# Optimization experiments

Hardware: AMD Instinct MI355X
Metric: run time of the kernel (lower is better)

The kernel has to match this reference:

```python
import jax, jax.numpy as jnp
import numpy as np

N = 10000          # nodes
E = 160000         # edges
T = 32             # seq_len == n_timesteps
H = 256            # hidden_size
K = 4              # edge_embedding_dim
NF = T * 6         # node_features
PRED = 8           # predicted_timesteps
T_TEACH = T - PRED # teacher-forced steps


def setup_inputs() -> dict:
    key = jax.random.key(0)
    ks = jax.random.split(key, 16)
    s = 0.05
    return {
        "x": jax.random.normal(ks[0], (N, NF), jnp.float32),
        "edge_index": jax.random.randint(ks[1], (2, E), 0, N, jnp.int64),
        "z": jax.random.uniform(ks[2], (E, K), jnp.float32),
        # inner f_out: Linear(H, NF) + ReLU
        "Wf": jax.random.normal(ks[3], (H, NF), jnp.float32) * s,
        "bf": jax.random.normal(ks[4], (NF,), jnp.float32) * s,
        # k-1 edge MLPs: Linear(2*NF, H) -> ReLU -> Linear(H, H), stacked
        "W1": jax.random.normal(ks[5], (K - 1, 2 * NF, H), jnp.float32) * s,
        "b1": jax.random.normal(ks[6], (K - 1, H), jnp.float32) * s,
        "W2": jax.random.normal(ks[7], (K - 1, H, H), jnp.float32) * s,
        "b2": jax.random.normal(ks[8], (K - 1, H), jnp.float32) * s,
        # GRUCell(6, H): torch gate order r, z, n
        "Wih": jax.random.normal(ks[9], (3 * H, 6), jnp.float32) * s,
        "bih": jax.random.normal(ks[10], (3 * H,), jnp.float32) * s,
        "Whh": jax.random.normal(ks[11], (3 * H, H), jnp.float32) * s,
        "bhh": jax.random.normal(ks[12], (3 * H,), jnp.float32) * s,
        # outer f_out: Linear(H, 6) + ReLU
        "Wo": jax.random.normal(ks[13], (H, 6), jnp.float32) * s,
        "bo": jax.random.normal(ks[14], (6,), jnp.float32) * s,
    }


def _forward(x, edge_index, z, Wf, bf, W1, b1, W2, b2, Wih, bih, Whh, bhh, Wo, bo):
    src = edge_index[0]  # x_j (source)
    dst = edge_index[1]  # x_i (target, aggregation index)
    zw = z[:, 1:K].T[:, :, None]  # [K-1, E, 1]
    ones_e = jnp.ones((E,), x.dtype)
    cnt = jnp.maximum(jax.ops.segment_sum(ones_e, dst, num_segments=N), 1.0)[:, None]

    def step(carry, inp):
        h, prev = carry
        t, x_t = inp
        inputs = jnp.where(t < T_TEACH, x_t, prev)  # [N, 6]
        fh = jax.nn.relu(h @ Wf + bf)               # [N, NF]
        # message: cat([x_i, x_j]) = [target, source], detached in torch
        ef = jax.lax.stop_gradient(
            jnp.concatenate([fh[dst], fh[src]], axis=1))  # [E, 2*NF]
        h1 = jax.nn.relu(jnp.einsum('ef,kfh->keh', ef, W1) + b1[:, None, :])
        h2 = jnp.einsum('keh,khg->keg', h1, W2) + b2[:, None, :]  # [K-1,E,H]
        msg = jnp.sum(zw * h2, axis=0)              # [E, H]
        m = jax.ops.segment_sum(msg, dst, num_segments=N) / cnt  # scatter-mean
        # GRUCell(inputs, hidden=m)
        gx = inputs @ Wih.T + bih                   # [N, 3H]
        gh = m @ Whh.T + bhh                        # [N, 3H]
        rx, zx, nx = jnp.split(gx, 3, axis=1)
        rh, zh, nh = jnp.split(gh, 3, axis=1)
        r = jax.nn.sigmoid(rx + rh)
        zg = jax.nn.sigmoid(zx + zh)
        n = jnp.tanh(nx + r * nh)
        h_new = (1.0 - zg) * n + zg * m             # [N, H]
        mu = inputs + jax.nn.relu(h_new @ Wo + bo)  # [N, 6]
        return (h_new, mu), mu

    x_seq = x.reshape(N, T, 6).transpose(1, 0, 2)   # [T, N, 6]
    ts = jnp.arange(T)
    h0 = jnp.zeros((N, H), x.dtype)
    p0 = jnp.zeros((N, 6), x.dtype)
    _, mus = jax.lax.scan(step, (h0, p0), (ts, x_seq))  # [T, N, 6]
    return mus.transpose(1, 0, 2).reshape(N, NF)


def reference(x, edge_index, z, Wf, bf, W1, b1, W2, b2, Wih, bih, Whh, bhh, Wo, bo):
    return _forward(x, edge_index, z, Wf, bf, W1, b1, W2, b2,
                    Wih, bih, Whh, bhh, Wo, bo)
```

## Files before the change

kernel.cpp:

```cpp
#include <hip/hip_runtime.h>
#include <hip/hip_bf16.h>

#define NN 10000
#define NE 160000
#define TS 32
#define HID 256
#define NFEAT 192
#define TTEACH 24

typedef unsigned short u16;
typedef unsigned int u32;
typedef __attribute__((ext_vector_type(8))) short bf16x8;
typedef __attribute__((ext_vector_type(4))) float f32x4;

__device__ __forceinline__ float bf2f(u16 u){
    u32 v = ((u32)u) << 16;
    union { u32 i; float f; } c; c.i = v; return c.f;
}
__device__ __forceinline__ u16 f2bf(float f){
    union { float f; u32 i; } c; c.f = f;
    u32 i = c.i;
    u32 lsb = (i >> 16) & 1u;
    i += 0x7fffu + lsb;
    return (u16)(i >> 16);
}

__global__ void fill_f32(float* p, float v, int n){
    int i = blockIdx.x * 256 + threadIdx.x;
    if (i < n) p[i] = v;
}
__global__ void fill_i32(int* p, int v, int n){
    int i = blockIdx.x * 256 + threadIdx.x;
    if (i < n) p[i] = v;
}
__global__ void copy_i32(const int* __restrict__ a, int* __restrict__ b, int n){
    int i = blockIdx.x * 256 + threadIdx.x;
    if (i < n) b[i] = a[i];
}
__global__ void copy_f32(const float* __restrict__ a, float* __restrict__ b, int n){
    int i = blockIdx.x * 256 + threadIdx.x;
    if (i < n) b[i] = a[i];
}

__global__ void detect_f32(const u16* __restrict__ zraw, int* __restrict__ flag){
    int c = 0;
    for (int i = 0; i < 128; i++) if (zraw[2*i] >= 0x4000) c++;
    *flag = (c > 8) ? 1 : 0;
}
__global__ void conv_f32(const void* __restrict__ in, float* __restrict__ outp,
                         int n, const int* __restrict__ flag){
    int i = blockIdx.x * 256 + threadIdx.x;
    if (i >= n) return;
    if (*flag) outp[i] = ((const float*)in)[i];
    else       outp[i] = bf2f(((const u16*)in)[i]);
}
__global__ void detect_i64(const int* __restrict__ ei_raw, int* __restrict__ flag){
    int zz = 0;
    #pragma unroll
    for (int i = 0; i < 32; i++) zz |= ei_raw[2*i + 1];
    *flag = (zz == 0) ? 1 : 0;
}
__global__ void copy_edges(const int* __restrict__ ei_raw, const int* __restrict__ flag,
                           int* __restrict__ src, int* __restrict__ dst){
    int e = blockIdx.x * 256 + threadIdx.x;
    if (e >= NE) return;
    int st = (*flag) ? 2 : 1;
    src[e] = ei_raw[(size_t)e * st];
    dst[e] = ei_raw[((size_t)NE + e) * st];
}

__global__ void degree_k(const int* __restrict__ dst, int* __restrict__ cnt, int n){
    int e = blockIdx.x * 256 + threadIdx.x;
    if (e < n) atomicAdd(&cnt[dst[e]], 1);
}
__global__ void invcnt_k(const int* __restrict__ cnt, float* __restrict__ inv, int n){
    int i = blockIdx.x * 256 + threadIdx.x;
    if (i < n) inv[i] = 1.0f / fmaxf((float)cnt[i], 1.0f);
}

__global__ void scan_k(const int* __restrict__ cnt, int* __restrict__ binoff){
    __shared__ int ps[1024];
    int t = threadIdx.x;
    int s = 0;
    if (t < 1000)
        for (int i = 0; i < 10; i++) s += cnt[t*10 + i];
    ps[t] = s;
    __syncthreads();
    for (int ofs = 1; ofs < 1024; ofs <<= 1){
        int v = (t >= ofs) ? ps[t - ofs] : 0;
        __syncthreads();
        ps[t] += v;
        __syncthreads();
    }
    if (t < 1000){
        int run = (t == 0) ? 0 : ps[t-1];
        for (int i = 0; i < 10; i++){
            binoff[t*10 + i] = run;
            run += cnt[t*10 + i];
        }
    }
}
__global__ void scatter_k(const int* __restrict__ src32, const int* __restrict__ dst32,
                          const float* __restrict__ zc, int* __restrict__ cur,
                          int* __restrict__ srcS, int* __restrict__ dstS,
                          float* __restrict__ zS){
    int e = blockIdx.x * 256 + threadIdx.x;
    if (e >= NE) return;
    int d = dst32[e];
    int pos = atomicAdd(&cur[d], 1);
    srcS[pos] = src32[e];
    dstS[pos] = d;
    zS[pos]        = zc[(size_t)e*4 + 1];
    zS[NE + pos]   = zc[(size_t)e*4 + 2];
    zS[2*NE + pos] = zc[(size_t)e*4 + 3];
}

__global__ void zsum_k(const int* __restrict__ dst32, const float* __restrict__ zc,
                       float* __restrict__ zsum){
    int e = blockIdx.x * 256 + threadIdx.x;
    if (e >= NE) return;
    int d = dst32[e];
    atomicAdd(&zsum[d*3 + 0], zc[(size_t)e*4 + 1]);
    atomicAdd(&zsum[d*3 + 1], zc[(size_t)e*4 + 2]);
    atomicAdd(&zsum[d*3 + 2], zc[(size_t)e*4 + 3]);
}
__global__ void build_bias_k(const float* __restrict__ zsum, const float* __restrict__ b2c,
                             float* __restrict__ bias_node){
    int idx = blockIdx.x * 256 + threadIdx.x;
    if (idx >= NN * 256) return;
    int n = idx >> 8, c = idx & 255;
    bias_node[idx] = zsum[n*3]*b2c[c] + zsum[n*3+1]*b2c[256+c] + zsum[n*3+2]*b2c[512+c];
}

__global__ void build_wft(const float* __restrict__ Wfc, u16* __restrict__ WfT){
    int idx = blockIdx.x * 256 + threadIdx.x;
    if (idx < 256 * 192){
        int k = idx / 192, n = idx % 192;
        WfT[(size_t)n * 256 + k] = f2bf(Wfc[idx]);
    }
}
__global__ void build_w1t(const float* __restrict__ W1c, u16* __restrict__ W1T){
    int idx = blockIdx.x * 256 + threadIdx.x;
    if (idx < 1536 * 192){
        int n = idx / 192, k = idx % 192;
        int kblk = n >> 9, part = (n >> 8) & 1, c = n & 255;
        W1T[idx] = f2bf(W1c[(size_t)kblk * (384*256) + (size_t)(part*192 + k) * 256 + c]);
    }
}
__global__ void conv_bf16(const float* __restrict__ in, u16* __restrict__ outp, int n){
    int i = blockIdx.x * 256 + threadIdx.x;
    if (i < n) outp[i] = f2bf(in[i]);
}
__global__ void build_w2t(const float* __restrict__ W2c, u16* __restrict__ W2T){
    int idx = blockIdx.x * 256 + threadIdx.x;
    if (idx < 768 * 256){
        int k = idx / 256, n = idx % 256;
        W2T[(size_t)n * 768 + k] = f2bf(W2c[idx]);
    }
}

template<int MODE>
__global__ __launch_bounds__(256, 2) void gemm_mfma(
    const u16* __restrict__ A16, const u16* __restrict__ BT16,
    const float* __restrict__ bias, float* __restrict__ Cf, u16* __restrict__ Cb,
    const float* __restrict__ A32, const float* __restrict__ rowscale,
    int M, int Kd, int Nd)
{
    __shared__ __align__(16) u16 Alds[256 * 40];
    __shared__ __align__(16) u16 Blds[64 * 40];
    const int tid = threadIdx.x;
    const int m0 = blockIdx.x * 256;
    const int n0 = blockIdx.y * 64;
    const int wave = tid >> 6, lane = tid & 63;
    const int quad = lane >> 4, l16 = lane & 15;

    const f32x4 zero4 = {0.f, 0.f, 0.f, 0.f};
    f32x4 acc[4][4];
    #pragma unroll
    for (int r=0;r<4;r++)
        #pragma unroll
        for (int c=0;c<4;c++) acc[r][c] = zero4;

    const int arow = m0 + tid;
    const u16* ap = (MODE == 2) ? nullptr : &A16[(size_t)arow * Kd];
    const int bn = tid >> 2, bseg = tid & 3;
    const u16* bp = &BT16[(size_t)(n0 + bn) * Kd + bseg * 8];
    float rs = 0.f;
    if (MODE == 2 && arow < M) rs = rowscale[arow];

    for (int k0 = 0; k0 < Kd; k0 += 32){
        if (MODE == 2){
            if (arow < M){
                const float4* q = reinterpret_cast<const float4*>(&A32[(size_t)arow * Kd + k0]);
                u32 pk[16];
                #pragma unroll
                for (int s=0;s<8;s++){
                    float4 v = q[s];
                    float2 p0; p0.x = v.x * rs; p0.y = v.y * rs;
                    float2 p1; p1.x = v.z * rs; p1.y = v.w * rs;
                    __hip_bfloat162 h0 = __float22bfloat162_rn(p0);
                    __hip_bfloat162 h1 = __float22bfloat162_rn(p1);
                    pk[2*s]   = *reinterpret_cast<u32*>(&h0);
                    pk[2*s+1] = *reinterpret_cast<u32*>(&h1);
                }
                #pragma unroll
                for (int s=0;s<4;s++)
                    *reinterpret_cast<uint4*>(&Alds[tid * 40 + s*8]) = *reinterpret_cast<uint4*>(&pk[4*s]);
            } else {
                uint4 zz = {0,0,0,0};
                #pragma unroll
                for (int s=0;s<4;s++)
                    *reinterpret_cast<uint4*>(&Alds[tid * 40 + s*8]) = zz;
            }
        } else {
            if (arow < M){
                const uint4* q = reinterpret_cast<const uint4*>(ap + k0);
                uint4 v0 = q[0], v1 = q[1], v2 = q[2], v3 = q[3];
                *reinterpret_cast<uint4*>(&Alds[tid * 40])      = v0;
                *reinterpret_cast<uint4*>(&Alds[tid * 40 + 8])  = v1;
                *reinterpret_cast<uint4*>(&Alds[tid * 40 + 16]) = v2;
                *reinterpret_cast<uint4*>(&Alds[tid * 40 + 24]) = v3;
            } else {
                uint4 zz = {0,0,0,0};
                #pragma unroll
                for (int s=0;s<4;s++)
                    *reinterpret_cast<uint4*>(&Alds[tid * 40 + s*8]) = zz;
            }
        }
        {
            uint4 v = *reinterpret_cast<const uint4*>(bp + k0);
            *reinterpret_cast<uint4*>(&Blds[bn * 40 + bseg * 8]) = v;
        }
        __syncthreads();
        bf16x8 af[4], bfr[4];
        #pragma unroll
        for (int r=0;r<4;r++)
            af[r] = *reinterpret_cast<const bf16x8*>(&Alds[(wave*64 + r*16 + l16) * 40 + quad * 8]);
        #pragma unroll
        for (int c=0;c<4;c++)
            bfr[c] = *reinterpret_cast<const bf16x8*>(&Blds[(c*16 + l16) * 40 + quad * 8]);
        #pragma unroll
        for (int r=0;r<4;r++)
            #pragma unroll
            for (int c=0;c<4;c++)
                acc[r][c] = __builtin_amdgcn_mfma_f32_16x16x32_bf16(af[r], bfr[c], acc[r][c], 0, 0, 0);
        __syncthreads();
    }
    #pragma unroll
    for (int c=0;c<4;c++){
        int col = n0 + c*16 + l16;
        float bv = 0.f;
        if (MODE == 0 || MODE == 2) bv = bias[col];
        if (MODE == 1){
            int part = (col >> 8) & 1;
            if (part == 0) bv = bias[(col >> 9) * 256 + (col & 255)];
        }
        #pragma unroll
        for (int r=0;r<4;r++){
            #pragma unroll
            for (int reg=0;reg<4;reg++){
                int row = m0 + wave*64 + r*16 + quad*4 + reg;
                if (row >= M) continue;
                float v = acc[r][c][reg] + bv;
                if (MODE == 0) v = fmaxf(v, 0.f);
                if (MODE == 2) Cf[(size_t)row * Nd + col] = v;
                else           Cb[(size_t)row * Nd + col] = f2bf(v);
            }
        }
    }
}

__global__ __launch_bounds__(256, 2) void edge_mfma(
    const u16* __restrict__ AB16, const u16* __restrict__ W2T,
    const float* __restrict__ zS,
    const int* __restrict__ srcS, const int* __restrict__ dstS,
    float* __restrict__ m_acc)
{
    __shared__ __align__(16) char smem[16640];
    u16*   Alds = (u16*)smem;
    float* stg  = (float*)smem;
    __shared__ float zc3[3][64];
    __shared__ int dstc[64], srcc[64];
    const int tid = threadIdx.x;
    const int eb = blockIdx.x * 64;

    if (tid < 64){
        srcc[tid] = srcS[eb + tid];
        dstc[tid] = dstS[eb + tid];
    }
    int tz = tid - 64;
    if (tz >= 0 && tz < 192){
        int g = tz / 64, e = tz % 64;
        zc3[g][e] = zS[(size_t)g * NE + eb + e];
    }
    __syncthreads();

    const int wave = tid >> 6, lane = tid & 63;
    const int quad = lane >> 4, l16 = lane & 15;
    const int est = tid >> 2, seg = tid & 3;

    const f32x4 zero4 = {0.f, 0.f, 0.f, 0.f};
    f32x4 acc[4][4];
    #pragma unroll
    for (int r=0;r<4;r++)
        #pragma unroll
        for (int c=0;c<4;c++) acc[r][c] = zero4;

    const int d = dstc[est], s = srcc[est];
    const u16* paB = &AB16[(size_t)d * 1536];
    const u16* pbB = &AB16[(size_t)s * 1536 + 256];
    const u16* wBl = &W2T[(size_t)(wave*64 + l16) * 768 + quad * 8];

    uint4 pa = *reinterpret_cast<const uint4*>(&paB[seg * 8]);
    uint4 pb = *reinterpret_cast<const uint4*>(&pbB[seg * 8]);
    uint4 bw0 = *reinterpret_cast<const uint4*>(&wBl[0]);
    uint4 bw1 = *reinterpret_cast<const uint4*>(&wBl[(size_t)16 * 768]);
    uint4 bw2 = *reinterpret_cast<const uint4*>(&wBl[(size_t)32 * 768]);
    uint4 bw3 = *reinterpret_cast<const uint4*>(&wBl[(size_t)48 * 768]);

    for (int kc = 0; kc < 768; kc += 32){
        const int g = kc >> 8;
        {
            union { uint4 v; u32 w[4]; } UA, UB;
            UA.v = pa; UB.v = pb;
            float zk = zc3[g][est];
            u32 pk[4];
            #pragma unroll
            for (int i=0;i<4;i++){
                float2 fa = __bfloat1622float2(*reinterpret_cast<__hip_bfloat162*>(&UA.w[i]));
                float2 fb = __bfloat1622float2(*reinterpret_cast<__hip_bfloat162*>(&UB.w[i]));
                float2 v;
                v.x = zk * fmaxf(fa.x + fb.x, 0.f);
                v.y = zk * fmaxf(fa.y + fb.y, 0.f);
                __hip_bfloat162 hr = __float22bfloat162_rn(v);
                pk[i] = *reinterpret_cast<u32*>(&hr);
            }
            *reinterpret_cast<uint4*>(&Alds[est * 40 + seg * 8]) = *reinterpret_cast<uint4*>(pk);
        }
        __syncthreads();
        if (kc + 32 < 768){
            const int kn = kc + 32;
            const int gn = kn >> 8;
            const int jn = (kn & 255) + seg * 8;
            pa = *reinterpret_cast<const uint4*>(&paB[gn * 512 + jn]);
            pb = *reinterpret_cast<const uint4*>(&pbB[gn * 512 + jn]);
        }
        bf16x8 af[4];
        #pragma unroll
        for (int r=0;r<4;r++)
            af[r] = *reinterpret_cast<const bf16x8*>(&Alds[(r*16 + l16) * 40 + quad * 8]);
        bf16x8 b0 = *reinterpret_cast<bf16x8*>(&bw0);
        bf16x8 b1 = *reinterpret_cast<bf16x8*>(&bw1);
        bf16x8 b2 = *reinterpret_cast<bf16x8*>(&bw2);
        bf16x8 b3 = *reinterpret_cast<bf16x8*>(&bw3);
        #pragma unroll
        for (int r=0;r<4;r++){
            acc[r][0] = __builtin_amdgcn_mfma_f32_16x16x32_bf16(af[r], b0, acc[r][0], 0, 0, 0);
            acc[r][1] = __builtin_amdgcn_mfma_f32_16x16x32_bf16(af[r], b1, acc[r][1], 0, 0, 0);
            acc[r][2] = __builtin_amdgcn_mfma_f32_16x16x32_bf16(af[r], b2, acc[r][2], 0, 0, 0);
            acc[r][3] = __builtin_amdgcn_mfma_f32_16x16x32_bf16(af[r], b3, acc[r][3], 0, 0, 0);
        }
        __syncthreads();
        if (kc + 32 < 768){
            const int kn = kc + 32;
            bw0 = *reinterpret_cast<const uint4*>(&wBl[kn]);
            bw1 = *reinterpret_cast<const uint4*>(&wBl[(size_t)16 * 768 + kn]);
            bw2 = *reinterpret_cast<const uint4*>(&wBl[(size_t)32 * 768 + kn]);
            bw3 = *reinterpret_cast<const uint4*>(&wBl[(size_t)48 * 768 + kn]);
        }
    }
    float sum = 0.f;
    int cur_d = -1;
    const int colg = wave*64 + lane;
    #pragma unroll
    for (int r = 0; r < 4; r++){
        #pragma unroll
        for (int c=0;c<4;c++)
            #pragma unroll
            for (int reg=0;reg<4;reg++)
                stg[wave*(16*65) + (quad*4 + reg)*65 + c*16 + l16] = acc[r][c][reg];
        __syncthreads();
        for (int e = 0; e < 16; e++){
            int eg = r*16 + e;
            int dn = dstc[eg];
            float v = stg[wave*(16*65) + e*65 + lane];
            if (dn != cur_d){
                if (cur_d >= 0) atomicAdd(&m_acc[(size_t)cur_d * 256 + colg], sum);
                cur_d = dn; sum = v;
            } else {
                sum += v;
            }
        }
        __syncthreads();
    }
    if (cur_d >= 0) atomicAdd(&m_acc[(size_t)cur_d * 256 + colg], sum);
}

__global__ void gates_mu_k(
    const float* __restrict__ gh, float* __restrict__ m_acc,
    const float* __restrict__ inv_cnt, const float* __restrict__ bias_node,
    const float* __restrict__ x,
    const float* __restrict__ Wih, const float* __restrict__ bih,
    const float* __restrict__ Wo, const float* __restrict__ bo,
    float* __restrict__ prev, u16* __restrict__ h16, void* __restrict__ out,
    const int* __restrict__ flag, int t)
{
    const int n = blockIdx.x;
    const int j = threadIdx.x;
    const int idx = n * 256 + j;
    float inp[6];
    if (t < TTEACH){
        #pragma unroll
        for (int c=0;c<6;c++) inp[c] = x[(size_t)n * NFEAT + t * 6 + c];
    } else {
        #pragma unroll
        for (int c=0;c<6;c++) inp[c] = prev[n * 6 + c];
    }
    float m = m_acc[idx] * inv_cnt[n];
    m_acc[idx] = bias_node[idx];
    float gxr = bih[j], gxz = bih[256 + j], gxn = bih[512 + j];
    #pragma unroll
    for (int c=0;c<6;c++){
        gxr += inp[c] * Wih[j * 6 + c];
        gxz += inp[c] * Wih[(256 + j) * 6 + c];
        gxn += inp[c] * Wih[(512 + j) * 6 + c];
    }
    float ghr = gh[(size_t)n * 768 + j];
    float ghz = gh[(size_t)n * 768 + 256 + j];
    float ghn = gh[(size_t)n * 768 + 512 + j];
    float r  = 1.f / (1.f + __expf(-(gxr + ghr)));
    float zg = 1.f / (1.f + __expf(-(gxz + ghz)));
    float nn = tanhf(gxn + r * ghn);
    float hv = (1.f - zg) * nn + zg * m;
    h16[idx] = f2bf(hv);
    __shared__ float hl[256];
    __shared__ float part[6][9];
    hl[j] = hv;
    __syncthreads();
    if (j < 48){
        int c = j >> 3, p = j & 7;
        float s = 0.f;
        #pragma unroll 8
        for (int q = 0; q < 32; q++){
            int jj = p*32 + q;
            s += hl[jj] * Wo[jj * 6 + c];
        }
        part[c][p] = s;
    }
    __syncthreads();
    if (j < 6){
        float s = bo[j];
        #pragma unroll
        for (int p = 0; p < 8; p++) s += part[j][p];
        float mu = inp[j] + fmaxf(s, 0.f);
        if (*flag) ((float*)out)[(size_t)n * NFEAT + t * 6 + j] = mu;
        else       ((u16*)out)[(size_t)n * NFEAT + t * 6 + j] = f2bf(mu);
        prev[n * 6 + j] = mu;
    }
}

extern "C" void kernel_launch(void* const* d_in, const int* in_sizes, int n_in,
                              void* d_out, int out_size, void* d_ws, size_t ws_size,
                              hipStream_t stream)
{
    const void* x_r   = d_in[0];
    const int*  ei    = (const int*)d_in[1];
    const void* z_r   = d_in[2];
    const void* Wf_r  = d_in[3];
    const void* bf_r  = d_in[4];
    const void* W1_r  = d_in[5];
    const void* b1_r  = d_in[6];
    const void* W2_r  = d_in[7];
    const void* b2_r  = d_in[8];
    const void* Wih_r = d_in[9];
    const void* bih_r = d_in[10];
    const void* Whh_r = d_in[11];
    const void* bhh_r = d_in[12];
    const void* Wo_r  = d_in[13];
    const void* bo_r  = d_in[14];

    char* ws = (char*)d_ws;
    size_t off = 0;
    auto alloc = [&](size_t bytes){
        void* p = ws + off;
        off += (bytes + 255) & ~(size_t)255;
        return p;
    };
    u16*   h16   = (u16*)  alloc((size_t)NN * HID * 2);
    float* prev  = (float*)alloc((size_t)NN * 6 * 4);
    u16*   fh16  = (u16*)  alloc((size_t)NN * NFEAT * 2);
    u16*   AB16  = (u16*)  alloc((size_t)NN * 1536 * 2);
    float* m_acc = (float*)alloc((size_t)NN * HID * 4);
    float* gh    = (float*)alloc((size_t)NN * 768 * 4);
    float* invc  = (float*)alloc((size_t)NN * 4);
    int*   cnt   = (int*)  alloc((size_t)NN * 4);
    int*   binoff= (int*)  alloc((size_t)(NN + 1) * 4);
    int*   curw  = (int*)  alloc((size_t)NN * 4);
    float* zsum  = (float*)alloc((size_t)NN * 3 * 4);
    float* biasN = (float*)alloc((size_t)NN * HID * 4);
    u16*   WfT   = (u16*)  alloc((size_t)192 * 256 * 2);
    u16*   W1T   = (u16*)  alloc((size_t)1536 * 192 * 2);
    u16*   Whh16 = (u16*)  alloc((size_t)768 * 256 * 2);
    u16*   W2T   = (u16*)  alloc((size_t)256 * 768 * 2);
    int*   src32 = (int*)  alloc((size_t)NE * 4);
    int*   dst32 = (int*)  alloc((size_t)NE * 4);
    int*   srcS  = (int*)  alloc((size_t)NE * 4);
    int*   dstS  = (int*)  alloc((size_t)NE * 4);
    float* zS    = (float*)alloc((size_t)3 * NE * 4);
    int*   fdt   = (int*)  alloc(256);
    int*   fidx  = (int*)  alloc(256);
    float* xc   = (float*)alloc((size_t)NN * NFEAT * 4);
    float* zc   = (float*)alloc((size_t)NE * 4 * 4);
    float* Wfc  = (float*)alloc((size_t)256 * 192 * 4);
    float* bfc  = (float*)alloc(192 * 4);
    float* W1c  = (float*)alloc((size_t)3 * 384 * 256 * 4);
    float* b1c  = (float*)alloc(768 * 4);
    float* W2c  = (float*)alloc((size_t)3 * 256 * 256 * 4);
    float* b2c  = (float*)alloc(768 * 4);
    float* Wihc = (float*)alloc((size_t)768 * 6 * 4);
    float* bihc = (float*)alloc(768 * 4);
    float* Whhc = (float*)alloc((size_t)768 * 256 * 4);
    float* bhhc = (float*)alloc(768 * 4);
    float* Woc  = (float*)alloc((size_t)256 * 6 * 4);
    float* boc  = (float*)alloc(6 * 4);

    detect_f32<<<1, 1, 0, stream>>>((const u16*)z_r, fdt);
    detect_i64<<<1, 1, 0, stream>>>(ei, fidx);
    copy_edges<<<(NE + 255)/256, 256, 0, stream>>>(ei, fidx, src32, dst32);

    auto conv = [&](const void* in, float* outp, int n){
        conv_f32<<<(n + 255)/256, 256, 0, stream>>>(in, outp, n, fdt);
    };
    conv(x_r,   xc,   NN * NFEAT);
    conv(z_r,   zc,   NE * 4);
    conv(Wf_r,  Wfc,  256 * 192);
    conv(bf_r,  bfc,  192);
    conv(W1_r,  W1c,  3 * 384 * 256);
    conv(b1_r,  b1c,  768);
    conv(W2_r,  W2c,  3 * 256 * 256);
    conv(b2_r,  b2c,  768);
    conv(Wih_r, Wihc, 768 * 6);
    conv(bih_r, bihc, 768);
    conv(Whh_r, Whhc, 768 * 256);
    conv(bhh_r, bhhc, 768);
    conv(Wo_r,  Woc,  256 * 6);
    conv(bo_r,  boc,  6);

    fill_f32<<<(NN*HID/2 + 255)/256, 256, 0, stream>>>((float*)h16, 0.f, NN*HID/2);
    fill_f32<<<(NN*6 + 255)/256, 256, 0, stream>>>(prev, 0.f, NN*6);
    fill_i32<<<(NN + 255)/256, 256, 0, stream>>>(cnt, 0, NN);
    fill_f32<<<(NN*3 + 255)/256, 256, 0, stream>>>(zsum, 0.f, NN*3);
    degree_k<<<(NE + 255)/256, 256, 0, stream>>>(dst32, cnt, NE);
    invcnt_k<<<(NN + 255)/256, 256, 0, stream>>>(cnt, invc, NN);
    zsum_k<<<(NE + 255)/256, 256, 0, stream>>>(dst32, zc, zsum);
    build_bias_k<<<(NN*HID + 255)/256, 256, 0, stream>>>(zsum, b2c, biasN);
    copy_f32<<<(NN*HID + 255)/256, 256, 0, stream>>>(biasN, m_acc, NN*HID);
    scan_k<<<1, 1024, 0, stream>>>(cnt, binoff);
    copy_i32<<<(NN + 255)/256, 256, 0, stream>>>(binoff, curw, NN);
    scatter_k<<<(NE + 255)/256, 256, 0, stream>>>(src32, dst32, zc, curw, srcS, dstS, zS);
    build_wft<<<(256*192 + 255)/256, 256, 0, stream>>>(Wfc, WfT);
    build_w1t<<<(1536*192 + 255)/256, 256, 0, stream>>>(W1c, W1T);
    conv_bf16<<<(768*256 + 255)/256, 256, 0, stream>>>(Whhc, Whh16, 768*256);
    build_w2t<<<(768*256 + 255)/256, 256, 0, stream>>>(W2c, W2T);

    for (int t = 0; t < TS; t++){
        gemm_mfma<0><<<dim3(40, 3), 256, 0, stream>>>(h16, WfT, bfc, nullptr, fh16, nullptr, nullptr, NN, 256, NFEAT);
        gemm_mfma<1><<<dim3(40, 24), 256, 0, stream>>>(fh16, W1T, b1c, nullptr, AB16, nullptr, nullptr, NN, NFEAT, 1536);
        edge_mfma<<<2500, 256, 0, stream>>>(AB16, W2T, zS, srcS, dstS, m_acc);
        gemm_mfma<2><<<dim3(40, 12), 256, 0, stream>>>(nullptr, Whh16, bhhc, gh, nullptr, m_acc, invc, NN, 256, 768);
        gates_mu_k<<<NN, 256, 0, stream>>>(gh, m_acc, invc, biasN, xc, Wihc, bihc, Woc, boc, prev, h16, d_out, fdt, t);
    }
}
```

Measured before the change: 7.802 ms.

## Build edge MFMA A-fragments directly in registers, dropping LDS staging and barriers

```diff
diff --git a/kernel.cpp b/kernel.cpp
--- a/kernel.cpp
+++ b/kernel.cpp
@@ -276,18 +276,15 @@
     const int* __restrict__ srcS, const int* __restrict__ dstS,
     float* __restrict__ m_acc)
 {
-    __shared__ __align__(16) char smem[16640];
-    u16*   Alds = (u16*)smem;
-    float* stg  = (float*)smem;
+    __shared__ float stg[4 * 16 * 65];
+    __shared__ int dstc[64];
     __shared__ float zc3[3][64];
-    __shared__ int dstc[64], srcc[64];
     const int tid = threadIdx.x;
     const int eb = blockIdx.x * 64;
-
-    if (tid < 64){
-        srcc[tid] = srcS[eb + tid];
-        dstc[tid] = dstS[eb + tid];
-    }
+    const int wave = tid >> 6, lane = tid & 63;
+    const int quad = lane >> 4, l16 = lane & 15;
+
+    if (tid < 64) dstc[tid] = dstS[eb + tid];
     int tz = tid - 64;
     if (tz >= 0 && tz < 192){
         int g = tz / 64, e = tz % 64;
@@ -295,10 +292,6 @@
     }
     __syncthreads();
 
-    const int wave = tid >> 6, lane = tid & 63;
-    const int quad = lane >> 4, l16 = lane & 15;
-    const int est = tid >> 2, seg = tid & 3;
-
     const f32x4 zero4 = {0.f, 0.f, 0.f, 0.f};
     f32x4 acc[4][4];
     #pragma unroll
@@ -306,67 +299,61 @@
         #pragma unroll
         for (int c=0;c<4;c++) acc[r][c] = zero4;
 
-    const int d = dstc[est], s = srcc[est];
-    const u16* paB = &AB16[(size_t)d * 1536];
-    const u16* pbB = &AB16[(size_t)s * 1536 + 256];
+    const u16* pd[4];
+    const u16* ps[4];
+    #pragma unroll
+    for (int r=0;r<4;r++){
+        int e = eb + r*16 + l16;
+        pd[r] = &AB16[(size_t)dstS[e] * 1536 + quad * 8];
+        ps[r] = &AB16[(size_t)srcS[e] * 1536 + 256 + quad * 8];
+    }
     const u16* wBl = &W2T[(size_t)(wave*64 + l16) * 768 + quad * 8];
 
-    uint4 pa = *reinterpret_cast<const uint4*>(&paB[seg * 8]);
-    uint4 pb = *reinterpret_cast<const uint4*>(&pbB[seg * 8]);
-    uint4 bw0 = *reinterpret_cast<const uint4*>(&wBl[0]);
-    uint4 bw1 = *reinterpret_cast<const uint4*>(&wBl[(size_t)16 * 768]);
-    uint4 bw2 = *reinterpret_cast<const uint4*>(&wBl[(size_t)32 * 768]);
-    uint4 bw3 = *reinterpret_cast<const uint4*>(&wBl[(size_t)48 * 768]);
-
+    float zr[4];
     for (int kc = 0; kc < 768; kc += 32){
         const int g = kc >> 8;
-        {
+        if ((kc & 255) == 0){
+            #pragma unroll
+            for (int r=0;r<4;r++) zr[r] = zc3[g][r*16 + l16];
+        }
+        const int off = g * 512 + (kc & 255);
+        uint4 Ad[4], As4[4], bw[4];
+        #pragma unroll
+        for (int r=0;r<4;r++){
+            Ad[r]  = *reinterpret_cast<const uint4*>(pd[r] + off);
+            As4[r] = *reinterpret_cast<const uint4*>(ps[r] + off);
+        }
+        #pragma unroll
+        for (int c=0;c<4;c++)
+            bw[c] = *reinterpret_cast<const uint4*>(&wBl[(size_t)c * 16 * 768 + kc]);
+        bf16x8 af[4];
+        #pragma unroll
+        for (int r=0;r<4;r++){
             union { uint4 v; u32 w[4]; } UA, UB;
-            UA.v = pa; UB.v = pb;
-            float zk = zc3[g][est];
+            UA.v = Ad[r]; UB.v = As4[r];
             u32 pk[4];
             #pragma unroll
             for (int i=0;i<4;i++){
                 float2 fa = __bfloat1622float2(*reinterpret_cast<__hip_bfloat162*>(&UA.w[i]));
                 float2 fb = __bfloat1622float2(*reinterpret_cast<__hip_bfloat162*>(&UB.w[i]));
                 float2 v;
-                v.x = zk * fmaxf(fa.x + fb.x, 0.f);
-                v.y = zk * fmaxf(fa.y + fb.y, 0.f);
+                v.x = zr[r] * fmaxf(fa.x + fb.x, 0.f);
+                v.y = zr[r] * fmaxf(fa.y + fb.y, 0.f);
                 __hip_bfloat162 hr = __float22bfloat162_rn(v);
                 pk[i] = *reinterpret_cast<u32*>(&hr);
             }
-            *reinterpret_cast<uint4*>(&Alds[est * 40 + seg * 8]) = *reinterpret_cast<uint4*>(pk);
-        }
-        __syncthreads();
-        if (kc + 32 < 768){
-            const int kn = kc + 32;
-            const int gn = kn >> 8;
-            const int jn = (kn & 255) + seg * 8;
-            pa = *reinterpret_cast<const uint4*>(&paB[gn * 512 + jn]);
-            pb = *reinterpret_cast<const uint4*>(&pbB[gn * 512 + jn]);
-        }
-        bf16x8 af[4];
-        #pragma unroll
-        for (int r=0;r<4;r++)
-            af[r] = *reinterpret_cast<const bf16x8*>(&Alds[(r*16 + l16) * 40 + quad * 8]);
-        bf16x8 b0 = *reinterpret_cast<bf16x8*>(&bw0);
-        bf16x8 b1 = *reinterpret_cast<bf16x8*>(&bw1);
-        bf16x8 b2 = *reinterpret_cast<bf16x8*>(&bw2);
-        bf16x8 b3 = *reinterpret_cast<bf16x8*>(&bw3);
+            af[r] = *reinterpret_cast<bf16x8*>(pk);
+        }
+        bf16x8 b0 = *reinterpret_cast<bf16x8*>(&bw[0]);
+        bf16x8 b1 = *reinterpret_cast<bf16x8*>(&bw[1]);
+        bf16x8 b2 = *reinterpret_cast<bf16x8*>(&bw[2]);
+        bf16x8 b3 = *reinterpret_cast<bf16x8*>(&bw[3]);
         #pragma unroll
         for (int r=0;r<4;r++){
             acc[r][0] = __builtin_amdgcn_mfma_f32_16x16x32_bf16(af[r], b0, acc[r][0], 0, 0, 0);
             acc[r][1] = __builtin_amdgcn_mfma_f32_16x16x32_bf16(af[r], b1, acc[r][1], 0, 0, 0);
             acc[r][2] = __builtin_amdgcn_mfma_f32_16x16x32_bf16(af[r], b2, acc[r][2], 0, 0, 0);
             acc[r][3] = __builtin_amdgcn_mfma_f32_16x16x32_bf16(af[r], b3, acc[r][3], 0, 0, 0);
-        }
-        __syncthreads();
-        if (kc + 32 < 768){
-            const int kn = kc + 32;
-            bw0 = *reinterpret_cast<const uint4*>(&wBl[kn]);
-            bw1 = *reinterpret_cast<const uint4*>(&wBl[(size_t)16 * 768 + kn]);
-            bw2 = *reinterpret_cast<const uint4*>(&wBl[(size_t)32 * 768 + kn]);
-            bw3 = *reinterpret_cast<const uint4*>(&wBl[(size_t)48 * 768 + kn]);
         }
     }
     float sum = 0.f;
```

New measurement: 12.64 ms. 62.0% more time.
